# Optimization experiments

Hardware: AMD Instinct MI355X
Metric: run time of the kernel (lower is better)

Reference implementation:

```python
import jax, jax.numpy as jnp
import numpy as np

B, H, W, C = 2, 256, 256, 256
P0, P1 = 8, 8
R0, R1 = H // P0, W // P1            # 32, 32 -> 1024 global tokens
NH = 8
DH = C // NH
MID = 4 * C                          # mlp_ratio = 4
HD = C * P0 * P1                     # high_dim = 16384
EPS = 1e-5


def _rel_index(Wh, Ww):
    # standard Swin-style relative position index, shape (Wh*Ww, Wh*Ww)
    coords = np.stack(np.meshgrid(np.arange(Wh), np.arange(Ww), indexing='ij'))
    coords = coords.reshape(2, -1)
    rel = coords[:, :, None] - coords[:, None, :]          # 2, N, N
    rel = rel.transpose(1, 2, 0).astype(np.int64)
    rel[:, :, 0] += Wh - 1
    rel[:, :, 1] += Ww - 1
    rel[:, :, 0] *= 2 * Ww - 1
    return rel.sum(-1)

_RPI = _rel_index(R0, R1)            # global branch: window_size = patch_res


def _ln(x, g, b):
    m = jnp.mean(x, axis=-1, keepdims=True)
    v = jnp.mean((x - m) ** 2, axis=-1, keepdims=True)
    return (x - m) * jax.lax.rsqrt(v + EPS) * g + b


def setup_inputs() -> dict:
    key = jax.random.key(0)
    ks = jax.random.split(key, 12)
    s = 0.02
    n_rel = (2 * R0 - 1) * (2 * R1 - 1)
    return {
        'x': jax.random.normal(ks[0], (B, H, W, C), jnp.float32),
        'ln1_g': jnp.ones((C,), jnp.float32), 'ln1_b': jnp.zeros((C,), jnp.float32),
        'ln2_g': jnp.ones((C,), jnp.float32), 'ln2_b': jnp.zeros((C,), jnp.float32),
        'rpe_table': jax.random.normal(ks[1], (n_rel, NH), jnp.float32) * s,
        'w_down': jax.random.normal(ks[2], (C, HD), jnp.float32) * s,
        'b_down': jnp.zeros((C,), jnp.float32),
        'w_up': jax.random.normal(ks[3], (HD, C), jnp.float32) * s,
        'b_up': jnp.zeros((HD,), jnp.float32),
        'w_qkv': jax.random.normal(ks[4], (3 * C, C), jnp.float32) * s,
        'b_qkv': jnp.zeros((3 * C,), jnp.float32),
        'w_proj': jax.random.normal(ks[5], (C, C), jnp.float32) * s,
        'b_proj': jnp.zeros((C,), jnp.float32),
        'w_fc1': jax.random.normal(ks[6], (MID, C), jnp.float32) * s,
        'b_fc1': jnp.zeros((MID,), jnp.float32),
        'w_fc2': jax.random.normal(ks[7], (C, MID), jnp.float32) * s,
        'b_fc2': jnp.zeros((C,), jnp.float32),
    }


def _block(x, ln1_g, ln1_b, ln2_g, ln2_b, rpe_table, w_down, b_down, w_up, b_up,
           w_qkv, b_qkv, w_proj, b_proj, w_fc1, b_fc1, w_fc2, b_fc2):
    shortcut = x
    y = _ln(x, ln1_g, ln1_b)
    # unfold + rearrange 'B (C P0 P1) (R0 R1) -> B (R0 R1) (P0 P1 C)'
    y = y.reshape(B, R0, P0, R1, P1, C).transpose(0, 1, 3, 2, 4, 5)
    y = y.reshape(B, R0 * R1, HD)                       # (B, L, high_dim)
    y = y @ w_down.T + b_down                           # (B, L, C)
    # relative position bias (NH, L, L)
    rpe = rpe_table[_RPI].transpose(2, 0, 1)
    # windowed multi-head self-attention
    L = R0 * R1
    qkv = (y @ w_qkv.T + b_qkv).reshape(B, L, 3, NH, DH).transpose(2, 0, 3, 1, 4)
    q, k, v = qkv[0], qkv[1], qkv[2]                    # (B, NH, L, DH)
    scale = DH ** -0.5
    attn = jnp.einsum('bhnd,bhmd->bhnm', q, k) * scale + rpe
    attn = jax.nn.softmax(attn, axis=-1)
    o = jnp.einsum('bhnm,bhmd->bhnd', attn, v)
    o = o.transpose(0, 2, 1, 3).reshape(B, L, C)
    o = o @ w_proj.T + b_proj
    y = o @ w_up.T + b_up                               # (B, L, high_dim)
    # fold back: (B, R0, R1, P0, P1, C) -> (B, H, W, C)
    y = y.reshape(B, R0, R1, P0, P1, C).transpose(0, 1, 3, 2, 4, 5).reshape(B, H, W, C)
    x = shortcut + y
    h = _ln(x, ln2_g, ln2_b)
    h = jax.nn.gelu(h @ w_fc1.T + b_fc1, approximate=False) @ w_fc2.T + b_fc2
    return x + h


def reference(x, ln1_g, ln1_b, ln2_g, ln2_b, rpe_table, w_down, b_down, w_up, b_up,
              w_qkv, b_qkv, w_proj, b_proj, w_fc1, b_fc1, w_fc2, b_fc2):
    return _block(x, ln1_g, ln1_b, ln2_g, ln2_b, rpe_table, w_down, b_down, w_up,
                  b_up, w_qkv, b_qkv, w_proj, b_proj, w_fc1, b_fc1, w_fc2, b_fc2)
```

## Files before the change

kernel.cpp:

```cpp
#include <hip/hip_runtime.h>

typedef __attribute__((ext_vector_type(8))) __bf16 bf16x8;
typedef __attribute__((ext_vector_type(4))) float f32x4;

#define MFMA16(a, b, c) __builtin_amdgcn_mfma_f32_16x16x32_bf16((a), (b), (c), 0, 0, 0)

#define ASYNC16(g, l) __builtin_amdgcn_global_load_lds( \
    (const __attribute__((address_space(1))) unsigned int*)(g), \
    (__attribute__((address_space(3))) unsigned int*)(l), 16, 0, 0)

__device__ __forceinline__ unsigned short f2bf(float f) {
    return __builtin_bit_cast(unsigned short, (__bf16)f);
}

__device__ __forceinline__ float wave_sum(float v) {
#pragma unroll
    for (int off = 32; off; off >>= 1) v += __shfl_xor(v, off, 64);
    return v;
}

__device__ __forceinline__ float gelu_fast(float v) {
    float z = v * fmaf(v * v, 0.0713548162f, 1.5957691216f);
    float e = __expf(-z);
    return v * __builtin_amdgcn_rcpf(1.f + e);
}

__global__ __launch_bounds__(256) void k_pre(const float* __restrict__ wdown, const float* __restrict__ wup,
                                             const float* __restrict__ wqkv, const float* __restrict__ wproj,
                                             const float* __restrict__ wfc1, const float* __restrict__ wfc2,
                                             unsigned short* __restrict__ dwdown, unsigned short* __restrict__ dwup,
                                             unsigned short* __restrict__ dwqkv, unsigned short* __restrict__ dwproj,
                                             unsigned short* __restrict__ dwfc1, unsigned short* __restrict__ dwfc2,
                                             const float* __restrict__ x, const float* __restrict__ g,
                                             const float* __restrict__ b, unsigned short* __restrict__ xln) {
    int bid = blockIdx.x;
    if (bid < 8960) {
        int i = (bid * 256 + threadIdx.x) * 4;
        const float* s; unsigned short* d; int off;
        if (i < 4194304)      { s = wdown; d = dwdown; off = i; }
        else if (i < 8388608) { s = wup;   d = dwup;   off = i - 4194304; }
        else if (i < 8585216) { s = wqkv;  d = dwqkv;  off = i - 8388608; }
        else if (i < 8650752) { s = wproj; d = dwproj; off = i - 8585216; }
        else if (i < 8912896) { s = wfc1;  d = dwfc1;  off = i - 8650752; }
        else                  { s = wfc2;  d = dwfc2;  off = i - 8912896; }
        float4 v = *reinterpret_cast<const float4*>(s + off);
        ushort4 o;
        o.x = f2bf(v.x); o.y = f2bf(v.y); o.z = f2bf(v.z); o.w = f2bf(v.w);
        *reinterpret_cast<ushort4*>(d + off) = o;
    } else {
        int wave = threadIdx.x >> 6, lane = threadIdx.x & 63;
        long long pix = (long long)(bid - 8960) * 4 + wave;
        const float* row = x + pix * 256;
        float4 v = *reinterpret_cast<const float4*>(row + lane * 4);
        float s = v.x + v.y + v.z + v.w;
        float s2 = v.x * v.x + v.y * v.y + v.z * v.z + v.w * v.w;
        s = wave_sum(s); s2 = wave_sum(s2);
        float mean = s * (1.f / 256.f);
        float rstd = rsqrtf(s2 * (1.f / 256.f) - mean * mean + 1e-5f);
        float4 gg = *reinterpret_cast<const float4*>(g + lane * 4);
        float4 bb = *reinterpret_cast<const float4*>(b + lane * 4);
        ushort4 ov;
        ov.x = f2bf((v.x - mean) * rstd * gg.x + bb.x);
        ov.y = f2bf((v.y - mean) * rstd * gg.y + bb.y);
        ov.z = f2bf((v.z - mean) * rstd * gg.z + bb.z);
        ov.w = f2bf((v.w - mean) * rstd * gg.w + bb.w);
        *reinterpret_cast<ushort4*>(xln + pix * 256 + lane * 4) = ov;
    }
}

__global__ __launch_bounds__(256, 2) void k_gemm_down2(const unsigned short* __restrict__ xln,
                                                       const unsigned short* __restrict__ wd,
                                                       float* __restrict__ part) {
    __shared__ alignas(16) unsigned short As[128 * 64];
    __shared__ alignas(16) unsigned short Bs[128 * 64];
    int wave = threadIdx.x >> 6, lane = threadIdx.x & 63, quad = lane >> 4, l16 = lane & 15;
    int mt = blockIdx.x * 128, nt = blockIdx.y * 128, k0 = blockIdx.z * 1024;
    int wm = wave & 1, wn = wave >> 1;
    int srow = wave * 32 + (lane >> 3);
    int schunk = lane & 7;
    f32x4 acc[4][4] = {};
    for (int s = 0; s < 16; s++) {
        int kg = k0 + s * 64;
        int p0 = kg >> 11, p1 = (kg >> 8) & 7, cbase = kg & 255;
#pragma unroll
        for (int i = 0; i < 4; i++) {
            int row = srow + i * 8;
            int m = mt + row;
            int bb = m >> 10, r0 = (m >> 5) & 31, r1 = m & 31;
            int c = cbase + ((schunk ^ (row & 7)) << 3);
            const unsigned short* g = xln +
                ((((long long)(bb * 256 + r0 * 8 + p0)) * 256 + (r1 * 8 + p1)) << 8) + c;
            ASYNC16(g, &As[(wave * 32 + i * 8) * 64]);
        }
#pragma unroll
        for (int i = 0; i < 4; i++) {
            int row = srow + i * 8;
            int n = nt + row;
            const unsigned short* g = wd + (long long)n * 16384 + kg + ((schunk ^ (row & 7)) << 3);
            ASYNC16(g, &Bs[(wave * 32 + i * 8) * 64]);
        }
        __syncthreads();
#pragma unroll
        for (int sub = 0; sub < 2; sub++) {
            int c = sub * 4 + quad;
            bf16x8 af[4], bfr[4];
#pragma unroll
            for (int mi = 0; mi < 4; mi++) {
                int row = wm * 64 + mi * 16 + l16;
                af[mi] = *reinterpret_cast<const bf16x8*>(&As[row * 64 + ((c ^ (row & 7)) << 3)]);
            }
#pragma unroll
            for (int ni = 0; ni < 4; ni++) {
                int row = wn * 64 + ni * 16 + l16;
                bfr[ni] = *reinterpret_cast<const bf16x8*>(&Bs[row * 64 + ((c ^ (row & 7)) << 3)]);
            }
#pragma unroll
            for (int mi = 0; mi < 4; mi++)
#pragma unroll
                for (int ni = 0; ni < 4; ni++)
                    acc[mi][ni] = MFMA16(af[mi], bfr[ni], acc[mi][ni]);
        }
        __syncthreads();
    }
    float* pb = part + (long long)blockIdx.z * 524288;
#pragma unroll
    for (int mi = 0; mi < 4; mi++)
#pragma unroll
        for (int ni = 0; ni < 4; ni++) {
            int n = nt + wn * 64 + ni * 16 + l16;
#pragma unroll
            for (int r = 0; r < 4; r++) {
                int m = mt + wm * 64 + mi * 16 + quad * 4 + r;
                pb[(long long)m * 256 + n] = acc[mi][ni][r];
            }
        }
}

__global__ __launch_bounds__(256) void k_red(const float* __restrict__ part,
                                             const float* __restrict__ bd,
                                             unsigned short* __restrict__ y) {
    int i = (blockIdx.x * 256 + threadIdx.x) * 4;
    float4 s = {0.f, 0.f, 0.f, 0.f};
#pragma unroll
    for (int p = 0; p < 16; p++) {
        float4 v = *reinterpret_cast<const float4*>(part + (long long)p * 524288 + i);
        s.x += v.x; s.y += v.y; s.z += v.z; s.w += v.w;
    }
    int n = i & 255;
    float4 bb = *reinterpret_cast<const float4*>(bd + n);
    ushort4 o;
    o.x = f2bf(s.x + bb.x); o.y = f2bf(s.y + bb.y);
    o.z = f2bf(s.z + bb.z); o.w = f2bf(s.w + bb.w);
    *reinterpret_cast<ushort4*>(y + i) = o;
}

__global__ __launch_bounds__(256) void k_gemm_qkv(const unsigned short* __restrict__ yd,
                                                  const unsigned short* __restrict__ wq,
                                                  const float* __restrict__ bq,
                                                  unsigned short* __restrict__ q,
                                                  unsigned short* __restrict__ k,
                                                  unsigned short* __restrict__ vT) {
    int wave = threadIdx.x >> 6, lane = threadIdx.x & 63, quad = lane >> 4, l16 = lane & 15;
    int m0 = blockIdx.x * 64 + wave * 16;
    int n0 = blockIdx.y * 64;
    const unsigned short* arow = yd + (long long)(m0 + l16) * 256;
    f32x4 acc[4] = {};
    for (int kb = 0; kb < 256; kb += 32) {
        bf16x8 a = *reinterpret_cast<const bf16x8*>(arow + kb + quad * 8);
#pragma unroll
        for (int ni = 0; ni < 4; ni++) {
            bf16x8 bv = *reinterpret_cast<const bf16x8*>(wq + (long long)(n0 + ni * 16 + l16) * 256 + kb + quad * 8);
            acc[ni] = MFMA16(a, bv, acc[ni]);
        }
    }
#pragma unroll
    for (int ni = 0; ni < 4; ni++) {
        int n = n0 + ni * 16 + l16;
        float bias = bq[n];
        int t = n >> 8, h = (n >> 5) & 7, d = n & 31;
#pragma unroll
        for (int r = 0; r < 4; r++) {
            int m = m0 + quad * 4 + r;
            int bh = ((m >> 10) << 3) | h;
            int l = m & 1023;
            unsigned short val = f2bf(acc[ni][r] + bias);
            if (t == 0)      q[((long long)bh * 1024 + l) * 32 + d] = val;
            else if (t == 1) k[((long long)bh * 1024 + l) * 32 + d] = val;
            else             vT[((long long)bh * 32 + d) * 1024 + l] = val;
        }
    }
}

__global__ __launch_bounds__(256) void k_attn(const unsigned short* __restrict__ q,
                                              const unsigned short* __restrict__ k,
                                              const unsigned short* __restrict__ vT,
                                              const float* __restrict__ rpe,
                                              unsigned short* __restrict__ o) {
    __shared__ alignas(16) char Pl[4][16 * 128];
    int wave = threadIdx.x >> 6, lane = threadIdx.x & 63, quad = lane >> 4, l16 = lane & 15;
    int bh = blockIdx.y, h = bh & 7;
    int m0 = blockIdx.x * 64 + wave * 16;
    const unsigned short* qb = q + (long long)bh * 32768;
    const unsigned short* kb = k + (long long)bh * 32768;
    const unsigned short* vb = vT + (long long)bh * 32768;
    char* pl = Pl[wave];
    const float scale = 0.17677669529663687f;
    int qi = m0 + l16;
    int qi0 = qi >> 5, qi1 = qi & 31;
    bf16x8 bq = *reinterpret_cast<const bf16x8*>(qb + qi * 32 + quad * 8);
    f32x4 o0 = {0.f, 0.f, 0.f, 0.f}, o1 = {0.f, 0.f, 0.f, 0.f};
    float m_run = -3.0e38f, l_run = 0.f;
    int swz = (l16 & 7) << 4;
    for (int t = 0; t < 16; t++) {
        f32x4 st[4];
        __builtin_amdgcn_s_setprio(1);
#pragma unroll
        for (int ni = 0; ni < 4; ni++) {
            bf16x8 ak = *reinterpret_cast<const bf16x8*>(kb + (t * 64 + ni * 16 + l16) * 32 + quad * 8);
            f32x4 z = {0.f, 0.f, 0.f, 0.f};
            st[ni] = MFMA16(ak, bq, z);
        }
        __builtin_amdgcn_s_setprio(0);
        float vals[16];
        float tmax = -3.0e38f;
#pragma unroll
        for (int ni = 0; ni < 4; ni++)
#pragma unroll
            for (int r = 0; r < 4; r++) {
                int kj = t * 64 + ni * 16 + quad * 4 + r;
                int kj0 = kj >> 5, kj1 = kj & 31;
                int idx = (qi0 - kj0 + 31) * 63 + (qi1 - kj1 + 31);
                float sv = st[ni][r] * scale + rpe[idx * 8 + h];
                vals[ni * 4 + r] = sv;
                tmax = fmaxf(tmax, sv);
            }
        tmax = fmaxf(tmax, __shfl_xor(tmax, 16, 64));
        tmax = fmaxf(tmax, __shfl_xor(tmax, 32, 64));
        float m_new = fmaxf(m_run, tmax);
        float fac = __expf(m_run - m_new);
        float tsum = 0.f;
#pragma unroll
        for (int ni = 0; ni < 4; ni++) {
            ushort4 w4;
            float p0v = __expf(vals[ni * 4 + 0] - m_new);
            float p1v = __expf(vals[ni * 4 + 1] - m_new);
            float p2v = __expf(vals[ni * 4 + 2] - m_new);
            float p3v = __expf(vals[ni * 4 + 3] - m_new);
            tsum += p0v + p1v + p2v + p3v;
            w4.x = f2bf(p0v); w4.y = f2bf(p1v); w4.z = f2bf(p2v); w4.w = f2bf(p3v);
            *reinterpret_cast<ushort4*>(pl + l16 * 128 + ((ni * 32 + quad * 8) ^ swz)) = w4;
        }
        tsum += __shfl_xor(tsum, 16, 64);
        tsum += __shfl_xor(tsum, 32, 64);
        l_run = l_run * fac + tsum;
        m_run = m_new;
#pragma unroll
        for (int r = 0; r < 4; r++) { o0[r] *= fac; o1[r] *= fac; }
#pragma unroll
        for (int kk = 0; kk < 2; kk++) {
            bf16x8 pb = *reinterpret_cast<const bf16x8*>(pl + l16 * 128 + ((kk * 64 + quad * 16) ^ swz));
            bf16x8 av0 = *reinterpret_cast<const bf16x8*>(vb + (long long)(l16) * 1024 + t * 64 + kk * 32 + quad * 8);
            bf16x8 av1 = *reinterpret_cast<const bf16x8*>(vb + (long long)(16 + l16) * 1024 + t * 64 + kk * 32 + quad * 8);
            __builtin_amdgcn_s_setprio(1);
            o0 = MFMA16(av0, pb, o0);
            o1 = MFMA16(av1, pb, o1);
            __builtin_amdgcn_s_setprio(0);
        }
    }
    float inv = 1.f / l_run;
    int b_ = bh >> 3;
    long long base = ((long long)(b_ * 1024 + qi)) * 256 + h * 32;
    ushort4 w0, w1;
    w0.x = f2bf(o0[0] * inv); w0.y = f2bf(o0[1] * inv);
    w0.z = f2bf(o0[2] * inv); w0.w = f2bf(o0[3] * inv);
    w1.x = f2bf(o1[0] * inv); w1.y = f2bf(o1[1] * inv);
    w1.z = f2bf(o1[2] * inv); w1.w = f2bf(o1[3] * inv);
    *reinterpret_cast<ushort4*>(o + base + quad * 4) = w0;
    *reinterpret_cast<ushort4*>(o + base + 16 + quad * 4) = w1;
}

__global__ __launch_bounds__(256) void k_gemm_proj(const unsigned short* __restrict__ a_,
                                                   const unsigned short* __restrict__ w,
                                                   const float* __restrict__ bias,
                                                   unsigned short* __restrict__ y) {
    int wave = threadIdx.x >> 6, lane = threadIdx.x & 63, quad = lane >> 4, l16 = lane & 15;
    int m0 = blockIdx.x * 64 + wave * 16;
    int n0 = blockIdx.y * 64;
    const unsigned short* arow = a_ + (long long)(m0 + l16) * 256;
    f32x4 acc[4] = {};
    for (int kb = 0; kb < 256; kb += 32) {
        bf16x8 a = *reinterpret_cast<const bf16x8*>(arow + kb + quad * 8);
#pragma unroll
        for (int ni = 0; ni < 4; ni++) {
            bf16x8 bv = *reinterpret_cast<const bf16x8*>(w + (long long)(n0 + ni * 16 + l16) * 256 + kb + quad * 8);
            acc[ni] = MFMA16(a, bv, acc[ni]);
        }
    }
#pragma unroll
    for (int ni = 0; ni < 4; ni++) {
        int n = n0 + ni * 16 + l16;
        float bv = bias[n];
#pragma unroll
        for (int r = 0; r < 4; r++)
            y[(long long)(m0 + quad * 4 + r) * 256 + n] = f2bf(acc[ni][r] + bv);
    }
}

__global__ __launch_bounds__(256) void k_up_fold(const unsigned short* __restrict__ a_,
                                                 const unsigned short* __restrict__ w,
                                                 const float* __restrict__ bup,
                                                 const float* __restrict__ x,
                                                 float* __restrict__ out) {
    int wave = threadIdx.x >> 6, lane = threadIdx.x & 63, quad = lane >> 4, l16 = lane & 15;
    int m0 = blockIdx.x * 64 + wave * 16;
    int n0 = blockIdx.y * 64;
    const unsigned short* arow = a_ + (long long)(m0 + l16) * 256;
    f32x4 acc[4] = {};
    for (int kb = 0; kb < 256; kb += 32) {
        bf16x8 a = *reinterpret_cast<const bf16x8*>(arow + kb + quad * 8);
#pragma unroll
        for (int ni = 0; ni < 4; ni++) {
            bf16x8 bv = *reinterpret_cast<const bf16x8*>(w + (long long)(n0 + ni * 16 + l16) * 256 + kb + quad * 8);
            acc[ni] = MFMA16(a, bv, acc[ni]);
        }
    }
#pragma unroll
    for (int ni = 0; ni < 4; ni++) {
        int n = n0 + ni * 16 + l16;
        float bias = bup[n];
        int p0 = n >> 11, p1 = (n >> 8) & 7, c = n & 255;
#pragma unroll
        for (int r = 0; r < 4; r++) {
            int m = m0 + quad * 4 + r;
            int bb = m >> 10, r0 = (m >> 5) & 31, r1 = m & 31;
            long long addr = ((long long)bb << 24) + (long long)(r0 * 8 + p0) * 65536 + (r1 * 8 + p1) * 256 + c;
            out[addr] = x[addr] + acc[ni][r] + bias;
        }
    }
}

#define LP 264
__global__ __launch_bounds__(512, 4) void k_mlp(float* __restrict__ xio,
                                                const float* __restrict__ g2,
                                                const float* __restrict__ b2,
                                                const unsigned short* __restrict__ w1,
                                                const float* __restrict__ bfc1,
                                                const unsigned short* __restrict__ w2,
                                                const float* __restrict__ bfc2) {
    __shared__ unsigned short Aln[64 * LP];
    __shared__ unsigned short Hc[64 * LP];
    int wave = threadIdx.x >> 6, lane = threadIdx.x & 63, quad = lane >> 4, l16 = lane & 15;
    long long m0 = (long long)blockIdx.x * 64;
    float4 gg = *reinterpret_cast<const float4*>(g2 + lane * 4);
    float4 bb = *reinterpret_cast<const float4*>(b2 + lane * 4);
#pragma unroll
    for (int i = 0; i < 8; i++) {
        int p = wave * 8 + i;
        float4 v = *reinterpret_cast<const float4*>(xio + (m0 + p) * 256 + lane * 4);
        float s = v.x + v.y + v.z + v.w;
        float s2 = v.x * v.x + v.y * v.y + v.z * v.z + v.w * v.w;
        s = wave_sum(s); s2 = wave_sum(s2);
        float mean = s * (1.f / 256.f);
        float rstd = rsqrtf(s2 * (1.f / 256.f) - mean * mean + 1e-5f);
        ushort4 o;
        o.x = f2bf((v.x - mean) * rstd * gg.x + bb.x);
        o.y = f2bf((v.y - mean) * rstd * gg.y + bb.y);
        o.z = f2bf((v.z - mean) * rstd * gg.z + bb.z);
        o.w = f2bf((v.w - mean) * rstd * gg.w + bb.w);
        *reinterpret_cast<ushort4*>(&Aln[p * LP + lane * 4]) = o;
    }
    __syncthreads();
    f32x4 acc2[4][2] = {};
    for (int ch = 0; ch < 4; ch++) {
        f32x4 acc1[4][2] = {};
        for (int kb = 0; kb < 256; kb += 32) {
            bf16x8 af[4];
#pragma unroll
            for (int mi = 0; mi < 4; mi++)
                af[mi] = *reinterpret_cast<const bf16x8*>(&Aln[(mi * 16 + l16) * LP + kb + quad * 8]);
#pragma unroll
            for (int ni = 0; ni < 2; ni++) {
                bf16x8 bv = *reinterpret_cast<const bf16x8*>(w1 + (long long)(ch * 256 + wave * 32 + ni * 16 + l16) * 256 + kb + quad * 8);
                __builtin_amdgcn_s_setprio(1);
#pragma unroll
                for (int mi = 0; mi < 4; mi++)
                    acc1[mi][ni] = MFMA16(af[mi], bv, acc1[mi][ni]);
                __builtin_amdgcn_s_setprio(0);
            }
        }
#pragma unroll
        for (int ni = 0; ni < 2; ni++) {
            int n = ch * 256 + wave * 32 + ni * 16 + l16;
            float bias = bfc1[n];
            int col = wave * 32 + ni * 16 + l16;
#pragma unroll
            for (int mi = 0; mi < 4; mi++) {
#pragma unroll
                for (int r = 0; r < 4; r++) {
                    float vv = acc1[mi][ni][r] + bias;
                    Hc[(mi * 16 + quad * 4 + r) * LP + col] = f2bf(gelu_fast(vv));
                }
            }
        }
        __syncthreads();
        for (int kb = 0; kb < 256; kb += 32) {
            bf16x8 af[4];
#pragma unroll
            for (int mi = 0; mi < 4; mi++)
                af[mi] = *reinterpret_cast<const bf16x8*>(&Hc[(mi * 16 + l16) * LP + kb + quad * 8]);
#pragma unroll
            for (int ni = 0; ni < 2; ni++) {
                bf16x8 bv = *reinterpret_cast<const bf16x8*>(w2 + (long long)(wave * 32 + ni * 16 + l16) * 1024 + ch * 256 + kb + quad * 8);
                __builtin_amdgcn_s_setprio(1);
#pragma unroll
                for (int mi = 0; mi < 4; mi++)
                    acc2[mi][ni] = MFMA16(af[mi], bv, acc2[mi][ni]);
                __builtin_amdgcn_s_setprio(0);
            }
        }
        __syncthreads();
    }
#pragma unroll
    for (int ni = 0; ni < 2; ni++) {
        int n = wave * 32 + ni * 16 + l16;
        float bias = bfc2[n];
#pragma unroll
        for (int mi = 0; mi < 4; mi++) {
#pragma unroll
            for (int r = 0; r < 4; r++) {
                long long row = m0 + mi * 16 + quad * 4 + r;
                float xv = xio[row * 256 + n];
                xio[row * 256 + n] = xv + acc2[mi][ni][r] + bias;
            }
        }
    }
}

extern "C" void kernel_launch(void* const* d_in, const int* in_sizes, int n_in,
                              void* d_out, int out_size, void* d_ws, size_t ws_size,
                              hipStream_t stream) {
    const float* x      = (const float*)d_in[0];
    const float* ln1_g  = (const float*)d_in[1];
    const float* ln1_b  = (const float*)d_in[2];
    const float* ln2_g  = (const float*)d_in[3];
    const float* ln2_b  = (const float*)d_in[4];
    const float* rpe    = (const float*)d_in[5];
    const float* w_down = (const float*)d_in[6];
    const float* b_down = (const float*)d_in[7];
    const float* w_up   = (const float*)d_in[8];
    const float* b_up   = (const float*)d_in[9];
    const float* w_qkv  = (const float*)d_in[10];
    const float* b_qkv  = (const float*)d_in[11];
    const float* w_proj = (const float*)d_in[12];
    const float* b_proj = (const float*)d_in[13];
    const float* w_fc1  = (const float*)d_in[14];
    const float* b_fc1  = (const float*)d_in[15];
    const float* w_fc2  = (const float*)d_in[16];
    const float* b_fc2  = (const float*)d_in[17];
    float* out = (float*)d_out;

    char* wp = (char*)d_ws;
    auto alloc = [&](size_t bytes) { void* p = (void*)wp; wp += (bytes + 255) & ~(size_t)255; return p; };
    unsigned short* wdown_bf = (unsigned short*)alloc(4194304 * 2);
    unsigned short* wup_bf   = (unsigned short*)alloc(4194304 * 2);
    unsigned short* wqkv_bf  = (unsigned short*)alloc(196608 * 2);
    unsigned short* wproj_bf = (unsigned short*)alloc(65536 * 2);
    unsigned short* wfc1_bf  = (unsigned short*)alloc(262144 * 2);
    unsigned short* wfc2_bf  = (unsigned short*)alloc(262144 * 2);
    unsigned short* ydown    = (unsigned short*)alloc(524288 * 2);
    unsigned short* qb       = (unsigned short*)alloc(524288 * 2);
    unsigned short* kb       = (unsigned short*)alloc(524288 * 2);
    unsigned short* vT       = (unsigned short*)alloc(524288 * 2);
    unsigned short* obf      = (unsigned short*)alloc(524288 * 2);
    unsigned short* oproj    = (unsigned short*)alloc(524288 * 2);

    unsigned short* xln = (unsigned short*)d_out;
    float* part         = (float*)((char*)d_out + 100663296);

    k_pre<<<41728, 256, 0, stream>>>(w_down, w_up, w_qkv, w_proj, w_fc1, w_fc2,
                                     wdown_bf, wup_bf, wqkv_bf, wproj_bf, wfc1_bf, wfc2_bf,
                                     x, ln1_g, ln1_b, xln);
    k_gemm_down2<<<dim3(16, 2, 16), 256, 0, stream>>>(xln, wdown_bf, part);
    k_red<<<512, 256, 0, stream>>>(part, b_down, ydown);
    k_gemm_qkv<<<dim3(32, 12), 256, 0, stream>>>(ydown, wqkv_bf, b_qkv, qb, kb, vT);
    k_attn<<<dim3(16, 16), 256, 0, stream>>>(qb, kb, vT, rpe, obf);
    k_gemm_proj<<<dim3(32, 4), 256, 0, stream>>>(obf, wproj_bf, b_proj, oproj);
    k_up_fold<<<dim3(32, 256), 256, 0, stream>>>(oproj, wup_bf, b_up, x, out);
    k_mlp<<<2048, 512, 0, stream>>>(out, ln2_g, ln2_b, wfc1_bf, b_fc1, wfc2_bf, b_fc2);
}
```

Before: 607.8 us.

## Stage up-projection weight tile in LDS and reuse it across 512 rows

The up-projection+fold kernel now loads a 128-column slice of the bf16 w_up into shared memory once per block, using async global-to-LDS copies with an XOR swizzle, and loops over 512 token rows. Previously every 64x64 block re-read weight rows straight from global memory. Staging the tile cuts redundant weight traffic and makes each block's per-thread tile larger (8 accumulators). The grid shrinks to 512 blocks and each block uses 64KB of LDS, which may lower occupancy. The kernel is dominated by the strided fp32 read/write of x/out (128MB), so the gain may be limited.

```diff
diff --git a/kernel.cpp b/kernel.cpp
--- a/kernel.cpp
+++ b/kernel.cpp
@@ -311,30 +311,48 @@
                                                  const float* __restrict__ bup,
                                                  const float* __restrict__ x,
                                                  float* __restrict__ out) {
+    __shared__ alignas(16) unsigned short Bs[128 * 256];
     int wave = threadIdx.x >> 6, lane = threadIdx.x & 63, quad = lane >> 4, l16 = lane & 15;
-    int m0 = blockIdx.x * 64 + wave * 16;
-    int n0 = blockIdx.y * 64;
-    const unsigned short* arow = a_ + (long long)(m0 + l16) * 256;
-    f32x4 acc[4] = {};
-    for (int kb = 0; kb < 256; kb += 32) {
-        bf16x8 a = *reinterpret_cast<const bf16x8*>(arow + kb + quad * 8);
-#pragma unroll
-        for (int ni = 0; ni < 4; ni++) {
-            bf16x8 bv = *reinterpret_cast<const bf16x8*>(w + (long long)(n0 + ni * 16 + l16) * 256 + kb + quad * 8);
-            acc[ni] = MFMA16(a, bv, acc[ni]);
-        }
-    }
-#pragma unroll
-    for (int ni = 0; ni < 4; ni++) {
-        int n = n0 + ni * 16 + l16;
-        float bias = bup[n];
-        int p0 = n >> 11, p1 = (n >> 8) & 7, c = n & 255;
-#pragma unroll
-        for (int r = 0; r < 4; r++) {
-            int m = m0 + quad * 4 + r;
-            int bb = m >> 10, r0 = (m >> 5) & 31, r1 = m & 31;
-            long long addr = ((long long)bb << 24) + (long long)(r0 * 8 + p0) * 65536 + (r1 * 8 + p1) * 256 + c;
-            out[addr] = x[addr] + acc[ni][r] + bias;
+    int n0 = blockIdx.x * 128;
+    int mbase = blockIdx.y * 512;
+#pragma unroll
+    for (int i = 0; i < 16; i++) {
+        int R = i * 8 + wave * 2;
+        int r = R + (lane >> 5);
+        int cg = (lane & 31) ^ (r & 7);
+        const unsigned short* g = w + (long long)(n0 + r) * 256 + cg * 8;
+        ASYNC16(g, &Bs[R * 256]);
+    }
+    __syncthreads();
+    float bias8[8];
+#pragma unroll
+    for (int ni = 0; ni < 8; ni++) bias8[ni] = bup[n0 + ni * 16 + l16];
+    for (int s = 0; s < 8; s++) {
+        int mr = mbase + s * 64 + wave * 16;
+        const unsigned short* arow = a_ + (long long)(mr + l16) * 256;
+        f32x4 acc[8] = {};
+#pragma unroll
+        for (int kb = 0; kb < 8; kb++) {
+            bf16x8 a = *reinterpret_cast<const bf16x8*>(arow + kb * 32 + quad * 8);
+#pragma unroll
+            for (int ni = 0; ni < 8; ni++) {
+                int nr = ni * 16 + l16;
+                bf16x8 bv = *reinterpret_cast<const bf16x8*>(
+                    &Bs[nr * 256 + (((kb * 4 + quad) ^ (nr & 7)) << 3)]);
+                acc[ni] = MFMA16(a, bv, acc[ni]);
+            }
+        }
+#pragma unroll
+        for (int ni = 0; ni < 8; ni++) {
+            int n = n0 + ni * 16 + l16;
+            int p0 = n >> 11, p1 = (n >> 8) & 7, c = n & 255;
+#pragma unroll
+            for (int r = 0; r < 4; r++) {
+                int m = mr + quad * 4 + r;
+                int bb = m >> 10, r0 = (m >> 5) & 31, r1 = m & 31;
+                long long addr = ((long long)bb << 24) + (long long)(r0 * 8 + p0) * 65536 + (r1 * 8 + p1) * 256 + c;
+                out[addr] = x[addr] + acc[ni][r] + bias8[ni];
+            }
         }
     }
 }
@@ -485,6 +503,6 @@
     k_gemm_qkv<<<dim3(32, 12), 256, 0, stream>>>(ydown, wqkv_bf, b_qkv, qb, kb, vT);
     k_attn<<<dim3(16, 16), 256, 0, stream>>>(qb, kb, vT, rpe, obf);
     k_gemm_proj<<<dim3(32, 4), 256, 0, stream>>>(obf, wproj_bf, b_proj, oproj);
-    k_up_fold<<<dim3(32, 256), 256, 0, stream>>>(oproj, wup_bf, b_up, x, out);
+    k_up_fold<<<dim3(128, 4), 256, 0, stream>>>(oproj, wup_bf, b_up, x, out);
     k_mlp<<<2048, 512, 0, stream>>>(out, ln2_g, ln2_b, wfc1_bf, b_fc1, wfc2_bf, b_fc2);
 }
```

New measurement: 506.3 us. 16.7% less time.
